# Kernel optimization log

Measured on AMD Instinct MI355X. Metric: run time of the kernel, lower is better.

Reference implementation:

```python
import jax, jax.numpy as jnp
import numpy as np

N, D, H = 524288, 64, 256


def setup_inputs() -> dict:
    key = jax.random.key(0)
    k1, k2, k3 = jax.random.split(key, 3)
    X = jax.random.normal(k1, (N, D), dtype=jnp.float32)
    centers = jax.random.normal(k2, (H, D), dtype=jnp.float32)
    w = jax.random.normal(k3, (1, H), dtype=jnp.float32) / np.sqrt(H)
    b = jnp.zeros((1,), dtype=jnp.float32)
    return {"X": X, "centers": centers, "w": w, "b": b}


def reference(X, centers, w, b):
    # RBF feature map: phi[n, h] = exp(-||X[n] - centers[h]||^2)
    # Squared euclidean distance via the expanded form to avoid the
    # [N, H, D] broadcast intermediate the naive torch version builds.
    x2 = jnp.sum(X * X, axis=-1, keepdims=True)           # [N, 1]
    c2 = jnp.sum(centers * centers, axis=-1)               # [H]
    xc = jnp.einsum('nd,hd->nh', X, centers)               # [N, H]
    d2 = jnp.maximum(x2 - 2.0 * xc + c2[None, :], 0.0)     # [N, H]
    feats = jnp.exp(-d2)                                   # gaussian kernel
    # Linear head: nn.Linear(hidden_dim, 1)
    return feats @ w.T + b                                 # [N, 1]
```

## Files before the change

### kernel.cpp

```cpp
#include <hip/hip_runtime.h>

#define NROWS 524288
#define DDIM  64
#define HCENT 256
#define GRID  512
#define CPB   4

typedef _Float16 half8 __attribute__((ext_vector_type(8)));
typedef float    f32x4 __attribute__((ext_vector_type(4)));

#define LOG2E 1.4426950408889634f
#define K2L   2.8853900817779268f
#define BIASF 80.0f

__device__ __forceinline__ float fast_exp2(float x) {
#if __has_builtin(__builtin_amdgcn_exp2f)
  return __builtin_amdgcn_exp2f(x);
#else
  return exp2f(x);
#endif
}

__global__ __launch_bounds__(512, 4) void rbf_main(const float* __restrict__ X,
                                                   const float* __restrict__ bptr,
                                                   const float* __restrict__ centers,
                                                   const float* __restrict__ w,
                                                   float* __restrict__ out);

__device__ __forceinline__ void load_chunk(const float* __restrict__ X, int rowbase,
                                           int c, int q, float4 (&raw)[8]) {
#pragma unroll
  for (int rt = 0; rt < 2; ++rt) {
    const float* rp = X + (rowbase + rt * 16 + c) * DDIM + q * 8;
#pragma unroll
    for (int kc = 0; kc < 2; ++kc) {
      raw[rt * 4 + kc * 2 + 0] = reinterpret_cast<const float4*>(rp + kc * 32)[0];
      raw[rt * 4 + kc * 2 + 1] = reinterpret_cast<const float4*>(rp + kc * 32)[1];
    }
  }
}

__device__ __forceinline__ void convert_chunk(const float4 (&raw)[8],
                                              half8 (&a)[2][2], float (&x2p)[2]) {
#pragma unroll
  for (int rt = 0; rt < 2; ++rt) {
    float part = 0.f;
#pragma unroll
    for (int kc = 0; kc < 2; ++kc) {
      const float4 f0 = raw[rt * 4 + kc * 2 + 0];
      const float4 f1 = raw[rt * 4 + kc * 2 + 1];
      const float xs[8] = {f0.x, f0.y, f0.z, f0.w, f1.x, f1.y, f1.z, f1.w};
      union { _Float16 h[8]; half8 v; } u;
#pragma unroll
      for (int p = 0; p < 8; ++p) {
        part = fmaf(xs[p], xs[p], part);
        u.h[p] = (_Float16)xs[p];
      }
      a[rt][kc] = u.v;
    }
    x2p[rt] = part;
  }
}

__device__ __forceinline__ void chunk_body(const float* __restrict__ X, int rowbase,
                                           bool prefetch,
                                           const float4 (&cur)[8], float4 (&nxt)[8],
                                           const half8* __restrict__ BHv,
                                           const float2* __restrict__ CWs,
                                           int lane, int q, int c, float bval,
                                           float* __restrict__ out) {
  if (prefetch) load_chunk(X, rowbase + 256, c, q, nxt);

  half8 a[2][2];
  float x2p[2];
  convert_chunk(cur, a, x2p);

  float psum[2][4] = {{0.f, 0.f, 0.f, 0.f}, {0.f, 0.f, 0.f, 0.f}};
#pragma unroll 2
  for (int ct = 0; ct < 16; ++ct) {
    int idx = ct * 128 + lane;
    half8 bh0 = BHv[idx], bh1 = BHv[idx + 64];
    float2 mw = CWs[ct * 16 + c];
#pragma unroll
    for (int rt = 0; rt < 2; ++rt) {
      f32x4 acc = {0.f, 0.f, 0.f, 0.f};
      acc = __builtin_amdgcn_mfma_f32_16x16x32_f16(a[rt][0], bh0, acc, 0, 0, 0);
      acc = __builtin_amdgcn_mfma_f32_16x16x32_f16(a[rt][1], bh1, acc, 0, 0, 0);
#pragma unroll
      for (int r = 0; r < 4; ++r) {
        float e = fast_exp2(fmaf(acc[r], K2L, mw.x));
        psum[rt][r] = fmaf(e, mw.y, psum[rt][r]);
      }
    }
  }

#pragma unroll
  for (int rt = 0; rt < 2; ++rt) {
    float part = x2p[rt];
    part += __shfl_xor(part, 16, 64);
    part += __shfl_xor(part, 32, 64);
#pragma unroll
    for (int r = 0; r < 4; ++r) {
      float v = psum[rt][r];
      v += __shfl_xor(v, 1, 64);
      v += __shfl_xor(v, 2, 64);
      v += __shfl_xor(v, 4, 64);
      v += __shfl_xor(v, 8, 64);
      float x2row = __shfl(part, q * 4 + r, 64);
      float rowf = fast_exp2(fmaf(-LOG2E, x2row, BIASF));
      psum[rt][r] = fmaf(v, rowf, bval);
    }
    if (c == 0) {
      float4 o = make_float4(psum[rt][0], psum[rt][1], psum[rt][2], psum[rt][3]);
      *reinterpret_cast<float4*>(out + rowbase + rt * 16 + q * 4) = o;
    }
  }
}

__global__ __launch_bounds__(512, 4) void rbf_main(const float* __restrict__ X,
                                                   const float* __restrict__ bptr,
                                                   const float* __restrict__ centers,
                                                   const float* __restrict__ w,
                                                   float* __restrict__ out) {
  __shared__ int4 BH[16 * 2 * 64];
  __shared__ float2 CWs[HCENT];

  const int tid  = threadIdx.x;
  const int wave = tid >> 6;
  const int lane = tid & 63;
  const int q    = lane >> 4;
  const int c    = lane & 15;

  float c2acc[2] = {0.f, 0.f};
#pragma unroll
  for (int i = 0; i < 4; ++i) {
    int pair = wave * 4 + i;
    int ct = pair >> 1;
    int kc = pair & 1;
    const float* src = centers + (ct * 16 + c) * DDIM + kc * 32 + q * 8;
    float4 f0 = reinterpret_cast<const float4*>(src)[0];
    float4 f1 = reinterpret_cast<const float4*>(src)[1];
    const float xs[8] = {f0.x, f0.y, f0.z, f0.w, f1.x, f1.y, f1.z, f1.w};
    union { _Float16 h[8]; int4 i4; } u;
    float part = 0.f;
#pragma unroll
    for (int p = 0; p < 8; ++p) {
      part = fmaf(xs[p], xs[p], part);
      u.h[p] = (_Float16)xs[p];
    }
    part += __shfl_xor(part, 16, 64);
    part += __shfl_xor(part, 32, 64);
    c2acc[i >> 1] += part;
    BH[pair * 64 + lane] = u.i4;
  }
  if (lane < 16) {
#pragma unroll
    for (int t = 0; t < 2; ++t) {
      int h = (wave * 2 + t) * 16 + lane;
      CWs[h] = make_float2(-fmaf(c2acc[t], LOG2E, BIASF), w[h]);
    }
  }

  float bval = bptr[0];

  __syncthreads();

  const half8* BHv = reinterpret_cast<const half8*>(BH);

  const int rb0 = blockIdx.x * CPB * 256 + wave * 32;

  float4 rawA[8], rawB[8];
  load_chunk(X, rb0, c, q, rawA);

  chunk_body(X, rb0 + 0 * 256, true,  rawA, rawB, BHv, CWs, lane, q, c, bval, out);
  chunk_body(X, rb0 + 1 * 256, true,  rawB, rawA, BHv, CWs, lane, q, c, bval, out);
  chunk_body(X, rb0 + 2 * 256, true,  rawA, rawB, BHv, CWs, lane, q, c, bval, out);
  chunk_body(X, rb0 + 3 * 256, false, rawB, rawA, BHv, CWs, lane, q, c, bval, out);
}

extern "C" void kernel_launch(void* const* d_in, const int* in_sizes, int n_in,
                              void* d_out, int out_size, void* d_ws, size_t ws_size,
                              hipStream_t stream) {
  const float* X       = (const float*)d_in[0];
  const float* centers = (const float*)d_in[1];
  const float* w       = (const float*)d_in[2];
  const float* b       = (const float*)d_in[3];
  float* out = (float*)d_out;
  (void)d_ws; (void)ws_size;

  rbf_main<<<GRID, 512, 0, stream>>>(X, b, centers, w, out);
}
```

Measured before the change: 205.0 us.

## Process one chunk per block with larger grid and drop register prefetch

Each block now handles a single 256-row chunk instead of four, so the grid grows from 512 to 2048 blocks. The software double-buffered register prefetch of X is removed, and launch bounds ask for 6 blocks per SM instead of 4. The aim is to lower register pressure, raise occupancy, and let hardware wave scheduling hide load latency rather than explicit prefetch. The cost is that every block rebuilds the fp16 centers table and center norms in shared memory, so that setup is repeated four times as often.

Result: slower. 212.5 us (+3.7%).

```diff
diff --git a/kernel.cpp b/kernel.cpp
--- a/kernel.cpp
+++ b/kernel.cpp
@@ -3,8 +3,7 @@
 #define NROWS 524288
 #define DDIM  64
 #define HCENT 256
-#define GRID  512
-#define CPB   4
+#define GRID  2048
 
 typedef _Float16 half8 __attribute__((ext_vector_type(8)));
 typedef float    f32x4 __attribute__((ext_vector_type(4)));
@@ -21,103 +20,7 @@
 #endif
 }
 
-__global__ __launch_bounds__(512, 4) void rbf_main(const float* __restrict__ X,
-                                                   const float* __restrict__ bptr,
-                                                   const float* __restrict__ centers,
-                                                   const float* __restrict__ w,
-                                                   float* __restrict__ out);
-
-__device__ __forceinline__ void load_chunk(const float* __restrict__ X, int rowbase,
-                                           int c, int q, float4 (&raw)[8]) {
-#pragma unroll
-  for (int rt = 0; rt < 2; ++rt) {
-    const float* rp = X + (rowbase + rt * 16 + c) * DDIM + q * 8;
-#pragma unroll
-    for (int kc = 0; kc < 2; ++kc) {
-      raw[rt * 4 + kc * 2 + 0] = reinterpret_cast<const float4*>(rp + kc * 32)[0];
-      raw[rt * 4 + kc * 2 + 1] = reinterpret_cast<const float4*>(rp + kc * 32)[1];
-    }
-  }
-}
-
-__device__ __forceinline__ void convert_chunk(const float4 (&raw)[8],
-                                              half8 (&a)[2][2], float (&x2p)[2]) {
-#pragma unroll
-  for (int rt = 0; rt < 2; ++rt) {
-    float part = 0.f;
-#pragma unroll
-    for (int kc = 0; kc < 2; ++kc) {
-      const float4 f0 = raw[rt * 4 + kc * 2 + 0];
-      const float4 f1 = raw[rt * 4 + kc * 2 + 1];
-      const float xs[8] = {f0.x, f0.y, f0.z, f0.w, f1.x, f1.y, f1.z, f1.w};
-      union { _Float16 h[8]; half8 v; } u;
-#pragma unroll
-      for (int p = 0; p < 8; ++p) {
-        part = fmaf(xs[p], xs[p], part);
-        u.h[p] = (_Float16)xs[p];
-      }
-      a[rt][kc] = u.v;
-    }
-    x2p[rt] = part;
-  }
-}
-
-__device__ __forceinline__ void chunk_body(const float* __restrict__ X, int rowbase,
-                                           bool prefetch,
-                                           const float4 (&cur)[8], float4 (&nxt)[8],
-                                           const half8* __restrict__ BHv,
-                                           const float2* __restrict__ CWs,
-                                           int lane, int q, int c, float bval,
-                                           float* __restrict__ out) {
-  if (prefetch) load_chunk(X, rowbase + 256, c, q, nxt);
-
-  half8 a[2][2];
-  float x2p[2];
-  convert_chunk(cur, a, x2p);
-
-  float psum[2][4] = {{0.f, 0.f, 0.f, 0.f}, {0.f, 0.f, 0.f, 0.f}};
-#pragma unroll 2
-  for (int ct = 0; ct < 16; ++ct) {
-    int idx = ct * 128 + lane;
-    half8 bh0 = BHv[idx], bh1 = BHv[idx + 64];
-    float2 mw = CWs[ct * 16 + c];
-#pragma unroll
-    for (int rt = 0; rt < 2; ++rt) {
-      f32x4 acc = {0.f, 0.f, 0.f, 0.f};
-      acc = __builtin_amdgcn_mfma_f32_16x16x32_f16(a[rt][0], bh0, acc, 0, 0, 0);
-      acc = __builtin_amdgcn_mfma_f32_16x16x32_f16(a[rt][1], bh1, acc, 0, 0, 0);
-#pragma unroll
-      for (int r = 0; r < 4; ++r) {
-        float e = fast_exp2(fmaf(acc[r], K2L, mw.x));
-        psum[rt][r] = fmaf(e, mw.y, psum[rt][r]);
-      }
-    }
-  }
-
-#pragma unroll
-  for (int rt = 0; rt < 2; ++rt) {
-    float part = x2p[rt];
-    part += __shfl_xor(part, 16, 64);
-    part += __shfl_xor(part, 32, 64);
-#pragma unroll
-    for (int r = 0; r < 4; ++r) {
-      float v = psum[rt][r];
-      v += __shfl_xor(v, 1, 64);
-      v += __shfl_xor(v, 2, 64);
-      v += __shfl_xor(v, 4, 64);
-      v += __shfl_xor(v, 8, 64);
-      float x2row = __shfl(part, q * 4 + r, 64);
-      float rowf = fast_exp2(fmaf(-LOG2E, x2row, BIASF));
-      psum[rt][r] = fmaf(v, rowf, bval);
-    }
-    if (c == 0) {
-      float4 o = make_float4(psum[rt][0], psum[rt][1], psum[rt][2], psum[rt][3]);
-      *reinterpret_cast<float4*>(out + rowbase + rt * 16 + q * 4) = o;
-    }
-  }
-}
-
-__global__ __launch_bounds__(512, 4) void rbf_main(const float* __restrict__ X,
+__global__ __launch_bounds__(512, 6) void rbf_main(const float* __restrict__ X,
                                                    const float* __restrict__ bptr,
                                                    const float* __restrict__ centers,
                                                    const float* __restrict__ w,
@@ -167,15 +70,76 @@
 
   const half8* BHv = reinterpret_cast<const half8*>(BH);
 
-  const int rb0 = blockIdx.x * CPB * 256 + wave * 32;
+  const int rowbase = blockIdx.x * 256 + wave * 32;
 
-  float4 rawA[8], rawB[8];
-  load_chunk(X, rb0, c, q, rawA);
+  half8 a[2][2];
+  float x2p[2];
+#pragma unroll
+  for (int rt = 0; rt < 2; ++rt) {
+    const float* rp = X + (rowbase + rt * 16 + c) * DDIM + q * 8;
+    float4 f[4];
+#pragma unroll
+    for (int kc = 0; kc < 2; ++kc) {
+      f[kc * 2 + 0] = reinterpret_cast<const float4*>(rp + kc * 32)[0];
+      f[kc * 2 + 1] = reinterpret_cast<const float4*>(rp + kc * 32)[1];
+    }
+    float part = 0.f;
+#pragma unroll
+    for (int kc = 0; kc < 2; ++kc) {
+      const float4 f0 = f[kc * 2 + 0];
+      const float4 f1 = f[kc * 2 + 1];
+      const float xs[8] = {f0.x, f0.y, f0.z, f0.w, f1.x, f1.y, f1.z, f1.w};
+      union { _Float16 h[8]; half8 v; } u;
+#pragma unroll
+      for (int p = 0; p < 8; ++p) {
+        part = fmaf(xs[p], xs[p], part);
+        u.h[p] = (_Float16)xs[p];
+      }
+      a[rt][kc] = u.v;
+    }
+    x2p[rt] = part;
+  }
 
-  chunk_body(X, rb0 + 0 * 256, true,  rawA, rawB, BHv, CWs, lane, q, c, bval, out);
-  chunk_body(X, rb0 + 1 * 256, true,  rawB, rawA, BHv, CWs, lane, q, c, bval, out);
-  chunk_body(X, rb0 + 2 * 256, true,  rawA, rawB, BHv, CWs, lane, q, c, bval, out);
-  chunk_body(X, rb0 + 3 * 256, false, rawB, rawA, BHv, CWs, lane, q, c, bval, out);
+  float psum[2][4] = {{0.f, 0.f, 0.f, 0.f}, {0.f, 0.f, 0.f, 0.f}};
+#pragma unroll 2
+  for (int ct = 0; ct < 16; ++ct) {
+    int idx = ct * 128 + lane;
+    half8 bh0 = BHv[idx], bh1 = BHv[idx + 64];
+    float2 mw = CWs[ct * 16 + c];
+#pragma unroll
+    for (int rt = 0; rt < 2; ++rt) {
+      f32x4 acc = {0.f, 0.f, 0.f, 0.f};
+      acc = __builtin_amdgcn_mfma_f32_16x16x32_f16(a[rt][0], bh0, acc, 0, 0, 0);
+      acc = __builtin_amdgcn_mfma_f32_16x16x32_f16(a[rt][1], bh1, acc, 0, 0, 0);
+#pragma unroll
+      for (int r = 0; r < 4; ++r) {
+        float e = fast_exp2(fmaf(acc[r], K2L, mw.x));
+        psum[rt][r] = fmaf(e, mw.y, psum[rt][r]);
+      }
+    }
+  }
+
+#pragma unroll
+  for (int rt = 0; rt < 2; ++rt) {
+    float part = x2p[rt];
+    part += __shfl_xor(part, 16, 64);
+    part += __shfl_xor(part, 32, 64);
+#pragma unroll
+    for (int r = 0; r < 4; ++r) {
+      float v = psum[rt][r];
+      v += __shfl_xor(v, 1, 64);
+      v += __shfl_xor(v, 2, 64);
+      v += __shfl_xor(v, 4, 64);
+      v += __shfl_xor(v, 8, 64);
+      float x2row = __shfl(part, q * 4 + r, 64);
+      float rowf = fast_exp2(fmaf(-LOG2E, x2row, BIASF));
+      psum[rt][r] = fmaf(v, rowf, bval);
+    }
+    if (c == 0) {
+      float4 o = make_float4(psum[rt][0], psum[rt][1], psum[rt][2], psum[rt][3]);
+      *reinterpret_cast<float4*>(out + rowbase + rt * 16 + q * 4) = o;
+    }
+  }
 }
 
 extern "C" void kernel_launch(void* const* d_in, const int* in_sizes, int n_in,
```
